# Performance work log

Measured on AMD Instinct MI355X. Metric: run time of the kernel, lower is better.

## Reference

```python
import jax, jax.numpy as jnp
import numpy as np
from jax import lax

DIM, HEADS, BS, TOPK, WIN = 256, 8, 8, 4, 7
HID = 2 * DIM  # DBFFN ffn_expansion_factor=2
B, H, W = 2, 56, 56


def _lin(x, w, b=None):
    # torch Linear: y = x @ W.T + b, W is [out, in]
    y = jnp.einsum('...c,oc->...o', x, w)
    return y if b is None else y + b


def _ln(x, w, b, eps=1e-6):
    mu = jnp.mean(x, -1, keepdims=True)
    var = jnp.mean((x - mu) ** 2, -1, keepdims=True)
    return (x - mu) * lax.rsqrt(var + eps) * w + b


def _mha(Q, K, V, wq_w, wq_b, wk_w, wk_b, wv_w, wv_b, p_w, p_b):
    # standard cross MHA: Q [B,Nq,C], K/V [B,Nk,C]
    Bq, Nq, C = Q.shape
    h, d = HEADS, C // HEADS
    scale = d ** -0.5
    q = _lin(Q, wq_w, wq_b).reshape(Bq, Nq, h, d)
    k = _lin(K, wk_w, wk_b).reshape(Bq, -1, h, d)
    v = _lin(V, wv_w, wv_b).reshape(Bq, -1, h, d)
    attn = jax.nn.softmax(jnp.einsum('bnhd,bmhd->bhnm', q, k) * scale, axis=-1)
    out = jnp.einsum('bhnm,bmhd->bnhd', attn, v).reshape(Bq, Nq, C)
    return _lin(out, p_w, p_b)


def setup_inputs() -> dict:
    key = jax.random.key(0)
    ks = jax.random.split(key, 16)
    s = 0.02
    C = DIM
    inp = {
        'x': jax.random.normal(ks[0], (B, C, H, W), jnp.float32),
        'pos_w': jax.random.normal(ks[1], (C, 1, 3, 3), jnp.float32) * s,
        'pos_b': jnp.zeros((C,), jnp.float32),
        'n1_w': jnp.ones((C,), jnp.float32), 'n1_b': jnp.zeros((C,), jnp.float32),
        'n2_w': jnp.ones((C,), jnp.float32), 'n2_b': jnp.zeros((C,), jnp.float32),
        'wq_w': jax.random.normal(ks[2], (3, C, C), jnp.float32) * s,
        'wq_b': jnp.zeros((3, C), jnp.float32),
        'wk_w': jax.random.normal(ks[3], (3, C, C), jnp.float32) * s,
        'wk_b': jnp.zeros((3, C), jnp.float32),
        'wv_w': jax.random.normal(ks[4], (3, C, C), jnp.float32) * s,
        'wv_b': jnp.zeros((3, C), jnp.float32),
        'pj_w': jax.random.normal(ks[5], (3, C, C), jnp.float32) * s,
        'pj_b': jnp.zeros((3, C), jnp.float32),
        # block scorer
        's1_w': jax.random.normal(ks[6], (C // 2, C), jnp.float32) * s,
        's1_b': jnp.zeros((C // 2,), jnp.float32),
        's2_w': jax.random.normal(ks[7], (1, C // 2), jnp.float32) * s,
        's2_b': jnp.zeros((1,), jnp.float32),
        # gating: per-token softmax weights over 3 branches
        'g_w': jax.random.normal(ks[8], (3, C), jnp.float32) * s,
        'g_b': jnp.zeros((3,), jnp.float32),
        # DBFFN (gated dconv FFN, bias=False): in-proj C->2*HID, dw 3x3, out-proj HID->C
        'pin_w': jax.random.normal(ks[9], (2 * HID, C), jnp.float32) * s,
        'dw_w': jax.random.normal(ks[10], (3, 3, 1, 2 * HID), jnp.float32) * s,
        'pout_w': jax.random.normal(ks[11], (C, HID), jnp.float32) * s,
    }
    return inp


def _forward(x, pos_w, pos_b, n1_w, n1_b, n2_w, n2_b, wq_w, wq_b, wk_w, wk_b,
             wv_w, wv_b, pj_w, pj_b, s1_w, s1_b, s2_w, s2_b, g_w, g_b,
             pin_w, dw_w, pout_w):
    Bx, C, Hx, Wx = x.shape
    # depthwise positional conv
    pos = lax.conv_general_dilated(x, pos_w, (1, 1), 'SAME',
                                   dimension_numbers=('NCHW', 'OIHW', 'NCHW'),
                                   feature_group_count=C)
    x = x + pos + pos_b[None, :, None, None] * 0 + pos_b[None, :, None, None]
    feat = jnp.transpose(x, (0, 2, 3, 1))  # NHWC
    Nq = Hx * Wx
    Q = feat.reshape(Bx, Nq, C)
    # block means
    nH, nW = Hx // BS, Wx // BS
    nB = nH * nW
    blk = feat.reshape(Bx, nH, BS, nW, BS, C).transpose(0, 1, 3, 2, 4, 5)
    blk = blk.reshape(Bx, nB, BS * BS, C).mean(axis=2)  # [B,nB,C]
    # block scores + top-k selection
    hsc = jax.nn.gelu(_lin(blk, s1_w, s1_b), approximate=False)
    scores = _lin(hsc, s2_w, s2_b)[..., 0]  # [B,nB]
    topk = min(TOPK, nB)
    _, idx = lax.top_k(scores, topk)
    K_sel = jnp.take_along_axis(blk, idx[:, :, None], axis=1)  # [B,topk,C]
    # compressed + selected branches
    y_cmp = _mha(Q, blk, blk, wq_w[0], wq_b[0], wk_w[0], wk_b[0], wv_w[0], wv_b[0], pj_w[0], pj_b[0])
    y_sel = _mha(Q, K_sel, K_sel, wq_w[1], wq_b[1], wk_w[1], wk_b[1], wv_w[1], wv_b[1], pj_w[1], pj_b[1])
    # local window branch (replicate-pad + unfold == shifted slices)
    pad = WIN // 2
    padded = jnp.pad(feat, ((0, 0), (pad, pad), (pad, pad), (0, 0)), mode='edge')
    patches = jnp.stack([padded[:, dy:dy + Hx, dx:dx + Wx, :]
                         for dy in range(WIN) for dx in range(WIN)], axis=3)
    patches = patches.reshape(Bx, Nq, WIN * WIN, C)  # [B,Nq,49,C]
    h, d = HEADS, C // HEADS
    scale = d ** -0.5
    q = _lin(Q, wq_w[2], wq_b[2]).reshape(Bx, Nq, h, d)
    k = _lin(patches, wk_w[2], wk_b[2]).reshape(Bx, Nq, WIN * WIN, h, d)
    v = _lin(patches, wv_w[2], wv_b[2]).reshape(Bx, Nq, WIN * WIN, h, d)
    attn = jax.nn.softmax(jnp.einsum('bnhd,bnwhd->bnhw', q, k) * scale, axis=-1)
    y_win = jnp.einsum('bnhw,bnwhd->bnhd', attn, v).reshape(Bx, Nq, C)
    y_win = _lin(y_win, pj_w[2], pj_b[2])
    # gated fusion + residual
    qn = _ln(Q, n1_w, n1_b)
    g = jax.nn.softmax(_lin(qn, g_w, g_b), axis=-1)  # [B,Nq,3]
    y = g[..., 0:1] * y_cmp + g[..., 1:2] * y_sel + g[..., 2:3] * y_win + Q
    ym = y.reshape(Bx, Hx, Wx, C)
    # DBFFN: gated depthwise-conv FFN (bias-free)
    t = _lin(ym, pin_w)  # [B,H,W,2*HID]
    t = lax.conv_general_dilated(t, dw_w, (1, 1), 'SAME',
                                 dimension_numbers=('NHWC', 'HWIO', 'NHWC'),
                                 feature_group_count=2 * HID)
    x1, x2 = jnp.split(t, 2, axis=-1)
    mlp = _lin(jax.nn.gelu(x1, approximate=False) * x2, pout_w)
    ym = _ln(ym + mlp, n2_w, n2_b)
    return jnp.transpose(ym, (0, 3, 1, 2))  # NCHW


def reference(x, pos_w, pos_b, n1_w, n1_b, n2_w, n2_b, wq_w, wq_b, wk_w, wk_b,
              wv_w, wv_b, pj_w, pj_b, s1_w, s1_b, s2_w, s2_b, g_w, g_b,
              pin_w, dw_w, pout_w):
    return _forward(x, pos_w, pos_b, n1_w, n1_b, n2_w, n2_b, wq_w, wq_b, wk_w,
                    wk_b, wv_w, wv_b, pj_w, pj_b, s1_w, s1_b, s2_w, s2_b,
                    g_w, g_b, pin_w, dw_w, pout_w)
```

## Files before the change

kernel.cpp:

```cpp
#include <hip/hip_runtime.h>

#define BATCH 2
#define CDIM 256
#define HEADS 8
#define HD 32
#define HH 56
#define WW 56
#define NQ 3136
#define NTOK 6272
#define NB 49
#define NTOPK 4
#define HID2 1024
#define HIDM 512
#define QSTRH 1280
#define ASTR 768

typedef short bf16x8 __attribute__((ext_vector_type(8)));
typedef float f32x4 __attribute__((ext_vector_type(4)));
typedef _Float16 h2 __attribute__((ext_vector_type(2)));
typedef _Float16 h4 __attribute__((ext_vector_type(4)));
struct __align__(16) h2x4 { h2 x, y, z, w; };

__device__ __forceinline__ float gelu_exact(float x) {
    return 0.5f * x * (1.f + erff(x * 0.70710678118654752f));
}

__device__ __forceinline__ short f2bf(float f) {
    union { float f; unsigned u; } v; v.f = f;
    unsigned r = v.u + 0x7FFFu + ((v.u >> 16) & 1u);
    return (short)(r >> 16);
}

__device__ __forceinline__ float fdot2h(h2 a, h2 b, float c) {
#if __has_builtin(__builtin_amdgcn_fdot2)
    return __builtin_amdgcn_fdot2(a, b, c, false);
#else
    return c + (float)a[0] * (float)b[0] + (float)a[1] * (float)b[1];
#endif
}

__device__ __forceinline__ void gld16(const void* gsrc, void* ldst) {
    __builtin_amdgcn_global_load_lds(
        (const __attribute__((address_space(1))) void*)gsrc,
        (__attribute__((address_space(3))) void*)ldst, 16, 0, 0);
}

__global__ __launch_bounds__(256) void k_init(
        const float* __restrict__ x, float* __restrict__ xT,
        const float* __restrict__ wq_w, const float* __restrict__ wk_w,
        const float* __restrict__ wv_w, const float* __restrict__ wq_b,
        const float* __restrict__ wk_b, const float* __restrict__ wv_b,
        const float* __restrict__ pj_w, const float* __restrict__ pin_w,
        const float* __restrict__ pout_w,
        short* __restrict__ Wc1, short* __restrict__ Wpj,
        short* __restrict__ Wpin, short* __restrict__ Wpout,
        float* __restrict__ bias1, float* __restrict__ Wkv0,
        float* __restrict__ bkv0, float* __restrict__ Wkv1,
        float* __restrict__ bkv1) {
    __shared__ float t[64][65];
    int bid = blockIdx.x;
    int tid = threadIdx.x;
    if (bid < 392) {
        int p0 = (bid % 49) * 64;
        int c0 = ((bid / 49) & 3) * 64;
        int b  = bid / 196;
        int pi = tid & 63, cj = tid >> 6;
        #pragma unroll
        for (int j = 0; j < 16; j++) {
            int c = cj * 16 + j;
            t[c][pi] = x[((size_t)(b * CDIM + c0 + c)) * NQ + p0 + pi];
        }
        __syncthreads();
        int ci = tid & 63, pj = tid >> 6;
        #pragma unroll
        for (int j = 0; j < 16; j++) {
            int p = pj * 16 + j;
            xT[((size_t)(b * NQ + p0 + p)) * CDIM + c0 + ci] = t[ci][p];
        }
        return;
    }
    int i = (bid - 392) * 256 + tid;
    if (i < 327680) {
        int r = i >> 8, k = i & 255, seg = r >> 8, n = r & 255;
        float v;
        if (seg == 0)      v = wq_w[n * 256 + k];
        else if (seg == 1) v = wq_w[65536 + n * 256 + k];
        else if (seg == 2) v = wq_w[131072 + n * 256 + k];
        else if (seg == 3) v = wk_w[131072 + n * 256 + k];
        else               v = wv_w[131072 + n * 256 + k];
        Wc1[i] = f2bf(v);
    } else if (i < 524288) {
        int j = i - 327680;
        int n = j / 768, tt = j % 768, br = tt >> 8, k = tt & 255;
        Wpj[j] = f2bf(pj_w[br * 65536 + n * 256 + k]);
    } else if (i < 786432) {
        int j = i - 524288;
        int r = j >> 8, k = j & 255;
        int o = (r & 3) * 256 + (r >> 2);
        Wpin[j] = f2bf(pin_w[o * 256 + k]);
    } else if (i < 917504) {
        int j = i - 786432;
        Wpout[j] = f2bf(pout_w[j]);
    } else if (i < 1048576) {
        int j = i - 917504;
        int r = j >> 8, k = j & 255;
        Wkv0[j] = (r < 256) ? wk_w[r * 256 + k] : wv_w[(r - 256) * 256 + k];
    } else if (i < 1179648) {
        int j = i - 1048576;
        int r = j >> 8, k = j & 255;
        Wkv1[j] = (r < 256) ? wk_w[65536 + r * 256 + k] : wv_w[65536 + (r - 256) * 256 + k];
    } else if (i < 1180928) {
        int j = i - 1179648;
        float v;
        if (j < 768)       v = wq_b[j];
        else if (j < 1024) v = wk_b[512 + (j - 768)];
        else               v = wv_b[512 + (j - 1024)];
        bias1[j] = v;
    } else if (i < 1181440) {
        int j = i - 1180928;
        bkv0[j] = (j < 256) ? wk_b[j] : wv_b[j - 256];
    } else if (i < 1181952) {
        int j = i - 1181440;
        bkv1[j] = (j < 256) ? wk_b[256 + j] : wv_b[j];
    }
}

__global__ __launch_bounds__(256) void k_posgates(
        const float* __restrict__ xT, const float* __restrict__ pw,
        const float* __restrict__ pb, const float* __restrict__ n1w,
        const float* __restrict__ n1b, const float* __restrict__ gw,
        const float* __restrict__ gb, float* __restrict__ feat,
        float* __restrict__ g, short* __restrict__ featb) {
    int wvid = threadIdx.x >> 6;
    int lane = threadIdx.x & 63;
    int c4 = lane * 4;
    float pwv[4][9];
    #pragma unroll
    for (int j = 0; j < 4; j++)
        #pragma unroll
        for (int i = 0; i < 9; i++) pwv[j][i] = pw[(c4 + j) * 9 + i];
    float4 pbv = *(const float4*)(pb + c4);
    float4 w1 = *(const float4*)(n1w + c4);
    float4 b1 = *(const float4*)(n1b + c4);
    float4 gw0 = *(const float4*)(gw + c4);
    float4 gw1 = *(const float4*)(gw + CDIM + c4);
    float4 gw2 = *(const float4*)(gw + 2 * CDIM + c4);
    float gb0 = gb[0], gb1 = gb[1], gb2 = gb[2];
    int tbase = blockIdx.x * 16 + wvid * 4;
    for (int t = 0; t < 4; t++) {
        int bn = tbase + t;
        int b = bn / NQ, n = bn % NQ;
        int y = n / WW, x = n % WW;
        const float* xb = xT + (size_t)b * NQ * CDIM;
        float4 a = *(const float4*)(xb + (size_t)n * CDIM + c4);
        float acc0 = a.x + pbv.x, acc1 = a.y + pbv.y;
        float acc2 = a.z + pbv.z, acc3 = a.w + pbv.w;
        #pragma unroll
        for (int dy = 0; dy < 3; dy++) {
            int yy = y + dy - 1;
            if (yy < 0 || yy >= HH) continue;
            #pragma unroll
            for (int dx = 0; dx < 3; dx++) {
                int xx = x + dx - 1;
                if (xx < 0 || xx >= WW) continue;
                float4 v = *(const float4*)(xb + ((size_t)(yy * WW + xx)) * CDIM + c4);
                int wi = dy * 3 + dx;
                acc0 += v.x * pwv[0][wi];
                acc1 += v.y * pwv[1][wi];
                acc2 += v.z * pwv[2][wi];
                acc3 += v.w * pwv[3][wi];
            }
        }
        *(float4*)(feat + (size_t)bn * CDIM + c4) = make_float4(acc0, acc1, acc2, acc3);
        short4 fb;
        fb.x = f2bf(acc0); fb.y = f2bf(acc1); fb.z = f2bf(acc2); fb.w = f2bf(acc3);
        *(short4*)(featb + (size_t)bn * CDIM + c4) = fb;
        float s = acc0 + acc1 + acc2 + acc3;
        #pragma unroll
        for (int off = 32; off > 0; off >>= 1) s += __shfl_xor(s, off);
        float mu = s * (1.f / CDIM);
        float d0 = acc0 - mu, d1 = acc1 - mu, d2 = acc2 - mu, d3 = acc3 - mu;
        float ss = d0 * d0 + d1 * d1 + d2 * d2 + d3 * d3;
        #pragma unroll
        for (int off = 32; off > 0; off >>= 1) ss += __shfl_xor(ss, off);
        float rstd = rsqrtf(ss * (1.f / CDIM) + 1e-6f);
        float q0 = d0 * rstd * w1.x + b1.x;
        float q1 = d1 * rstd * w1.y + b1.y;
        float q2 = d2 * rstd * w1.z + b1.z;
        float q3 = d3 * rstd * w1.w + b1.w;
        float p0 = q0 * gw0.x + q1 * gw0.y + q2 * gw0.z + q3 * gw0.w;
        float p1 = q0 * gw1.x + q1 * gw1.y + q2 * gw1.z + q3 * gw1.w;
        float p2 = q0 * gw2.x + q1 * gw2.y + q2 * gw2.z + q3 * gw2.w;
        #pragma unroll
        for (int off = 32; off > 0; off >>= 1) {
            p0 += __shfl_xor(p0, off);
            p1 += __shfl_xor(p1, off);
            p2 += __shfl_xor(p2, off);
        }
        if (lane == 0) {
            float l0 = p0 + gb0, l1 = p1 + gb1, l2 = p2 + gb2;
            float m3 = fmaxf(l0, fmaxf(l1, l2));
            float e0 = __expf(l0 - m3), e1 = __expf(l1 - m3), e2 = __expf(l2 - m3);
            float inv = 1.f / (e0 + e1 + e2);
            g[bn * 3 + 0] = e0 * inv;
            g[bn * 3 + 1] = e1 * inv;
            g[bn * 3 + 2] = e2 * inv;
        }
    }
}

__global__ __launch_bounds__(256) void k_blkscore(
        const float* __restrict__ feat, const float* __restrict__ s1w,
        const float* __restrict__ s1b, const float* __restrict__ s2w,
        const float* __restrict__ s2b, float* __restrict__ blk,
        float* __restrict__ scores) {
    __shared__ float sblk[256];
    __shared__ float red[128];
    int gid = blockIdx.x;
    int b = gid / NB, bid = gid % NB;
    int by = bid / 7, bx = bid % 7;
    int c = threadIdx.x;
    float s = 0.f;
    for (int iy = 0; iy < 8; iy++)
        for (int ix = 0; ix < 8; ix++) {
            int y = by * 8 + iy, xx = bx * 8 + ix;
            s += feat[((size_t)(b * NQ + y * WW + xx)) * CDIM + c];
        }
    s *= (1.f / 64.f);
    blk[(size_t)gid * CDIM + c] = s;
    sblk[c] = s;
    __syncthreads();
    if (c < 128) {
        const float* wrow = s1w + (size_t)c * CDIM;
        float acc = s1b[c];
        for (int k = 0; k < CDIM; k++) acc += sblk[k] * wrow[k];
        red[c] = gelu_exact(acc) * s2w[c];
    }
    __syncthreads();
    #pragma unroll
    for (int st = 64; st > 0; st >>= 1) {
        if (c < st) red[c] += red[c + st];
        __syncthreads();
    }
    if (c == 0) scores[gid] = red[0] + s2b[0];
}

__global__ __launch_bounds__(256) void k_gemm64kv(
        const float* __restrict__ blk, const float* __restrict__ Wkv0,
        const float* __restrict__ bkv0, _Float16* __restrict__ kvcmp,
        const float* __restrict__ scores, const float* __restrict__ Wkv1,
        const float* __restrict__ bkv1, _Float16* __restrict__ kvsel) {
    __shared__ float As[16][68];
    __shared__ float Ws[16][68];
    __shared__ float ssc[2][NB];
    __shared__ int sidx[8];
    const float* W; const float* bias; _Float16* C; int M;
    int m0;
    bool sel = (blockIdx.y == 2);
    if (!sel) { W = Wkv0; bias = bkv0; C = kvcmp; M = 98; m0 = blockIdx.y * 64; }
    else      { W = Wkv1; bias = bkv1; C = kvsel; M = 8;  m0 = 0; }
    const int N = 512, K = 256;
    const int tid = threadIdx.x;
    const int tx = tid & 15, ty = tid >> 4;
    const int n0 = blockIdx.x * 64;
    const int lr = tid >> 2;
    const int lk = (tid & 3) * 4;
    if (sel) {
        if (tid < 2 * NB) ssc[tid / NB][tid % NB] = scores[tid];
        __syncthreads();
        if (tid < 2) {
            for (int t = 0; t < NTOPK; t++) {
                int best = 0; float bv = -1e30f;
                for (int m = 0; m < NB; m++)
                    if (ssc[tid][m] > bv) { bv = ssc[tid][m]; best = m; }
                sidx[tid * 4 + t] = best; ssc[tid][best] = -1e30f;
            }
        }
        __syncthreads();
    }
    int gm = m0 + lr;
    int arow = gm;
    if (sel && gm < 8) arow = (gm >> 2) * NB + sidx[gm];
    float acc[4][4] = {};
    for (int k0 = 0; k0 < K; k0 += 16) {
        float4 av = make_float4(0.f, 0.f, 0.f, 0.f);
        if (gm < M) av = *(const float4*)(blk + (size_t)arow * K + k0 + lk);
        int gn = n0 + lr;
        float4 wv = make_float4(0.f, 0.f, 0.f, 0.f);
        if (gn < N) wv = *(const float4*)(W + (size_t)gn * K + k0 + lk);
        __syncthreads();
        As[lk][lr] = av.x; As[lk + 1][lr] = av.y; As[lk + 2][lr] = av.z; As[lk + 3][lr] = av.w;
        Ws[lk][lr] = wv.x; Ws[lk + 1][lr] = wv.y; Ws[lk + 2][lr] = wv.z; Ws[lk + 3][lr] = wv.w;
        __syncthreads();
        #pragma unroll
        for (int kk = 0; kk < 16; kk++) {
            const float4 a = *(const float4*)&As[kk][ty * 4];
            const float4 b = *(const float4*)&Ws[kk][tx * 4];
            acc[0][0] += a.x * b.x; acc[0][1] += a.x * b.y; acc[0][2] += a.x * b.z; acc[0][3] += a.x * b.w;
            acc[1][0] += a.y * b.x; acc[1][1] += a.y * b.y; acc[1][2] += a.y * b.z; acc[1][3] += a.y * b.w;
            acc[2][0] += a.z * b.x; acc[2][1] += a.z * b.y; acc[2][2] += a.z * b.z; acc[2][3] += a.z * b.w;
            acc[3][0] += a.w * b.x; acc[3][1] += a.w * b.y; acc[3][2] += a.w * b.z; acc[3][3] += a.w * b.w;
        }
    }
    #pragma unroll
    for (int i = 0; i < 4; i++) {
        int om = m0 + ty * 4 + i;
        if (om >= M) break;
        #pragma unroll
        for (int j = 0; j < 4; j++) {
            int gn = n0 + tx * 4 + j;
            C[(size_t)om * N + gn] = (_Float16)(acc[i][j] + bias[gn]);
        }
    }
}

__global__ __launch_bounds__(256) void k_gemm64x128(
        const short* __restrict__ A, const short* __restrict__ W,
        const float* __restrict__ bias, int M, int N, int K,
        _Float16* __restrict__ C2) {
    __shared__ short As[64][40];
    __shared__ short Bs[128][40];
    int tid = threadIdx.x;
    int wid = tid >> 6, lane = tid & 63;
    int wm = wid >> 1, wn = wid & 1;
    int m0 = blockIdx.y * 64, n0 = blockIdx.x * 128;
    f32x4 acc[2][4] = {};
    int ar = tid >> 2, ac = (tid & 3) * 8;
    int br = tid >> 1, bc = (tid & 1) * 16;
    int fr = lane & 15, fk = (lane >> 4) * 8;
    for (int k0 = 0; k0 < K; k0 += 32) {
        bf16x8 a0 = *(const bf16x8*)(A + (size_t)(m0 + ar) * K + k0 + ac);
        const short* wp = W + (size_t)(n0 + br) * K + k0 + bc;
        bf16x8 wv0 = *(const bf16x8*)(wp);
        bf16x8 wv1 = *(const bf16x8*)(wp + 8);
        __syncthreads();
        *(bf16x8*)&As[ar][ac] = a0;
        *(bf16x8*)&Bs[br][bc] = wv0;
        *(bf16x8*)&Bs[br][bc + 8] = wv1;
        __syncthreads();
        bf16x8 af[2], bf[4];
        #pragma unroll
        for (int mi = 0; mi < 2; mi++)
            af[mi] = *(const bf16x8*)&As[wm * 32 + mi * 16 + fr][fk];
        #pragma unroll
        for (int ni = 0; ni < 4; ni++)
            bf[ni] = *(const bf16x8*)&Bs[wn * 64 + ni * 16 + fr][fk];
        #pragma unroll
        for (int mi = 0; mi < 2; mi++)
            #pragma unroll
            for (int ni = 0; ni < 4; ni++)
                acc[mi][ni] = __builtin_amdgcn_mfma_f32_16x16x32_bf16(
                    af[mi], bf[ni], acc[mi][ni], 0, 0, 0);
    }
    int rsub = (lane >> 4) * 4;
    #pragma unroll
    for (int mi = 0; mi < 2; mi++) {
        #pragma unroll
        for (int ni = 0; ni < 4; ni++) {
            int col = n0 + wn * 64 + ni * 16 + (lane & 15);
            float bv = bias ? bias[col] : 0.f;
            #pragma unroll
            for (int r = 0; r < 4; r++) {
                int row = m0 + wm * 32 + mi * 16 + rsub + r;
                C2[(size_t)row * N + col] = (_Float16)(acc[mi][ni][r] + bv);
            }
        }
    }
}

__global__ __launch_bounds__(256) void k_gemm64(
        const short* __restrict__ A, const short* __restrict__ W,
        const float* __restrict__ bias, float* __restrict__ C,
        int M, int N, int K,
        const float* __restrict__ resid, const float* __restrict__ g3,
        const float* __restrict__ pjb, short* __restrict__ Cb) {
    __shared__ short As[64][40];
    __shared__ short Bs[64][40];
    int tid = threadIdx.x;
    int wid = tid >> 6, lane = tid & 63;
    int wm = wid >> 1, wn = wid & 1;
    int m0 = blockIdx.y * 64, n0 = blockIdx.x * 64;
    f32x4 acc[2][2] = {};
    int ar = tid >> 2, ac = (tid & 3) * 8;
    int fr = lane & 15, fk = (lane >> 4) * 8;
    for (int k0 = 0; k0 < K; k0 += 32) {
        bf16x8 a0 = *(const bf16x8*)(A + (size_t)(m0 + ar) * K + k0 + ac);
        bf16x8 w0 = *(const bf16x8*)(W + (size_t)(n0 + ar) * K + k0 + ac);
        __syncthreads();
        *(bf16x8*)&As[ar][ac] = a0;
        *(bf16x8*)&Bs[ar][ac] = w0;
        __syncthreads();
        bf16x8 af[2], bf[2];
        #pragma unroll
        for (int mi = 0; mi < 2; mi++)
            af[mi] = *(const bf16x8*)&As[wm * 32 + mi * 16 + fr][fk];
        #pragma unroll
        for (int ni = 0; ni < 2; ni++)
            bf[ni] = *(const bf16x8*)&Bs[wn * 32 + ni * 16 + fr][fk];
        #pragma unroll
        for (int mi = 0; mi < 2; mi++)
            #pragma unroll
            for (int ni = 0; ni < 2; ni++)
                acc[mi][ni] = __builtin_amdgcn_mfma_f32_16x16x32_bf16(
                    af[mi], bf[ni], acc[mi][ni], 0, 0, 0);
    }
    int rsub = (lane >> 4) * 4;
    #pragma unroll
    for (int mi = 0; mi < 2; mi++) {
        #pragma unroll
        for (int ni = 0; ni < 2; ni++) {
            int col = n0 + wn * 32 + ni * 16 + (lane & 15);
            #pragma unroll
            for (int r = 0; r < 4; r++) {
                int row = m0 + wm * 32 + mi * 16 + rsub + r;
                float v = acc[mi][ni][r];
                if (resid) {
                    v += resid[(size_t)row * N + col]
                       + g3[row * 3 + 0] * pjb[col]
                       + g3[row * 3 + 1] * pjb[256 + col]
                       + g3[row * 3 + 2] * pjb[512 + col];
                } else if (bias) {
                    v += bias[col];
                }
                C[(size_t)row * N + col] = v;
                if (Cb) Cb[(size_t)row * N + col] = f2bf(v);
            }
        }
    }
}

__global__ __launch_bounds__(512) void k_attn_lds(
        const _Float16* __restrict__ bufQ, const _Float16* __restrict__ kvc,
        const _Float16* __restrict__ kvs, short* __restrict__ Acatb,
        const float* __restrict__ g) {
    __shared__ uint4 buf[100 * 32];
    int tid = threadIdx.x;
    int wid = tid >> 6;
    int lane = tid & 63;
    int l = tid & 31;
    int tk = tid >> 5;
    int dg = l & 3;
    int co = l * 8;
    const float scale = 0.17677669529663687f;

    if (blockIdx.x < 392) {
        int bid = blockIdx.x;
        int swz = (bid & 7) * 49 + (bid >> 3);
        int t0 = swz * 16;
        int tok = t0 + tk;
        int b = t0 / NQ;
        const _Float16* kb = kvc + (size_t)b * NB * 512;
        for (int p = wid * 2; p < NB + 1; p += 16) {
            int myp = p + (lane >> 5);
            if (myp > NB - 1) myp = NB - 1;
            gld16((const uint4*)(kb + (size_t)myp * 512) + (lane & 31), &buf[p * 32]);
        }
        const _Float16* qrow = bufQ + (size_t)tok * QSTRH;
        float gate0 = g[tok * 3 + 0];
        float gate1 = g[tok * 3 + 1];
        short* orow = Acatb + (size_t)tok * ASTR;
        h2x4 qv = *(const h2x4*)(qrow + co);
        __syncthreads();
        float sc[13];
        sc[12] = -1e30f;
        #pragma unroll
        for (int m = 0; m < NB; m++) {
            h2x4 kv = *(const h2x4*)&buf[m * 32 + l];
            float acc = fdot2h(qv.x, kv.x, 0.f);
            acc = fdot2h(qv.y, kv.y, acc);
            acc = fdot2h(qv.z, kv.z, acc);
            acc = fdot2h(qv.w, kv.w, acc);
            acc += __shfl_xor(acc, 1);
            acc += __shfl_xor(acc, 2);
            if ((m & 3) == dg) sc[m >> 2] = acc * scale;
        }
        float mx = sc[0];
        #pragma unroll
        for (int i = 1; i < 13; i++) mx = fmaxf(mx, sc[i]);
        mx = fmaxf(mx, __shfl_xor(mx, 1));
        mx = fmaxf(mx, __shfl_xor(mx, 2));
        float sum = 0.f;
        #pragma unroll
        for (int i = 0; i < 13; i++) { sc[i] = __expf(sc[i] - mx); sum += sc[i]; }
        sum += __shfl_xor(sum, 1);
        sum += __shfl_xor(sum, 2);
        float inv_c = 1.f / sum;
        __syncthreads();
        for (int p = wid * 2; p < NB + 1; p += 16) {
            int myp = p + (lane >> 5);
            if (myp > NB - 1) myp = NB - 1;
            gld16((const uint4*)(kb + (size_t)myp * 512 + 256) + (lane & 31), &buf[p * 32]);
        }
        {
            const _Float16* ksb = kvs + (size_t)b * NTOPK * 512;
            h2x4 qs = *(const h2x4*)(qrow + 256 + co);
            float sv = 0.f;
            #pragma unroll
            for (int m = 0; m < NTOPK; m++) {
                h2x4 kk = *(const h2x4*)(ksb + (size_t)m * 512 + co);
                float acc = fdot2h(qs.x, kk.x, 0.f);
                acc = fdot2h(qs.y, kk.y, acc);
                acc = fdot2h(qs.z, kk.z, acc);
                acc = fdot2h(qs.w, kk.w, acc);
                acc += __shfl_xor(acc, 1);
                acc += __shfl_xor(acc, 2);
                if (m == dg) sv = acc * scale;
            }
            float mxs = sv;
            mxs = fmaxf(mxs, __shfl_xor(mxs, 1));
            mxs = fmaxf(mxs, __shfl_xor(mxs, 2));
            float e = __expf(sv - mxs);
            float sums = e;
            sums += __shfl_xor(sums, 1);
            sums += __shfl_xor(sums, 2);
            float invs = 1.f / sums;
            float o[8];
            #pragma unroll
            for (int d = 0; d < 8; d++) o[d] = 0.f;
            #pragma unroll
            for (int m = 0; m < NTOPK; m++) {
                float pw = __shfl(e, m, 4);
                h2x4 vv = *(const h2x4*)(ksb + (size_t)m * 512 + 256 + co);
                o[0] += pw * (float)vv.x[0]; o[1] += pw * (float)vv.x[1];
                o[2] += pw * (float)vv.y[0]; o[3] += pw * (float)vv.y[1];
                o[4] += pw * (float)vv.z[0]; o[5] += pw * (float)vv.z[1];
                o[6] += pw * (float)vv.w[0]; o[7] += pw * (float)vv.w[1];
            }
            float gg = gate1 * invs;
            bf16x8 ov;
            #pragma unroll
            for (int d = 0; d < 8; d++) ov[d] = f2bf(o[d] * gg);
            *(bf16x8*)(orow + 256 + co) = ov;
        }
        __syncthreads();
        {
            float o[8];
            #pragma unroll
            for (int d = 0; d < 8; d++) o[d] = 0.f;
            #pragma unroll
            for (int m = 0; m < NB; m++) {
                float pw = __shfl(sc[m >> 2], m & 3, 4);
                h2x4 vv = *(const h2x4*)&buf[m * 32 + l];
                o[0] += pw * (float)vv.x[0]; o[1] += pw * (float)vv.x[1];
                o[2] += pw * (float)vv.y[0]; o[3] += pw * (float)vv.y[1];
                o[4] += pw * (float)vv.z[0]; o[5] += pw * (float)vv.z[1];
                o[6] += pw * (float)vv.w[0]; o[7] += pw * (float)vv.w[1];
            }
            float gg = gate0 * inv_c;
            bf16x8 ov;
            #pragma unroll
            for (int d = 0; d < 8; d++) ov[d] = f2bf(o[d] * gg);
            *(bf16x8*)(orow + co) = ov;
        }
    } else {
        int bid = blockIdx.x - 392;
        int swz = (bid & 7) * 49 + (bid >> 3);
        int b = swz / 196;
        int r = swz % 196;
        int y0 = (r / 14) * 4;
        int x0 = (r % 14) * 4;
        int ty = tk >> 2, tx = tk & 3;
        int y = y0 + ty, x = x0 + tx;
        int tok = b * NQ + y * WW + x;
        const _Float16* KVb = bufQ + (size_t)b * NQ * QSTRH;
        for (int p = wid * 2; p < 100; p += 16) {
            int pp = p + (lane >> 5);
            int pr = pp / 10, pc = pp - pr * 10;
            int gy = min(max(y0 + pr - 3, 0), HH - 1);
            int gx = min(max(x0 + pc - 3, 0), WW - 1);
            gld16((const uint4*)(KVb + (size_t)(gy * WW + gx) * QSTRH + 768) + (lane & 31),
                  &buf[p * 32]);
        }
        h2x4 qv = *(const h2x4*)(bufQ + (size_t)tok * QSTRH + 512 + co);
        float gate = g[tok * 3 + 2];
        __syncthreads();
        float sw[13];
        sw[12] = -1e30f;
        #pragma unroll
        for (int dy = 0; dy < 7; dy++) {
            #pragma unroll
            for (int dx = 0; dx < 7; dx++) {
                int p = (ty + dy) * 10 + tx + dx;
                h2x4 kv = *(const h2x4*)&buf[p * 32 + l];
                float acc = fdot2h(qv.x, kv.x, 0.f);
                acc = fdot2h(qv.y, kv.y, acc);
                acc = fdot2h(qv.z, kv.z, acc);
                acc = fdot2h(qv.w, kv.w, acc);
                acc += __shfl_xor(acc, 1);
                acc += __shfl_xor(acc, 2);
                int m = dy * 7 + dx;
                if ((m & 3) == dg) sw[m >> 2] = acc * scale;
            }
        }
        float mx = sw[0];
        #pragma unroll
        for (int i = 1; i < 13; i++) mx = fmaxf(mx, sw[i]);
        mx = fmaxf(mx, __shfl_xor(mx, 1));
        mx = fmaxf(mx, __shfl_xor(mx, 2));
        float sum = 0.f;
        #pragma unroll
        for (int i = 0; i < 13; i++) { sw[i] = __expf(sw[i] - mx); sum += sw[i]; }
        sum += __shfl_xor(sum, 1);
        sum += __shfl_xor(sum, 2);
        float inv = 1.f / sum;
        __syncthreads();
        for (int p = wid * 2; p < 100; p += 16) {
            int pp = p + (lane >> 5);
            int pr = pp / 10, pc = pp - pr * 10;
            int gy = min(max(y0 + pr - 3, 0), HH - 1);
            int gx = min(max(x0 + pc - 3, 0), WW - 1);
            gld16((const uint4*)(KVb + (size_t)(gy * WW + gx) * QSTRH + 1024) + (lane & 31),
                  &buf[p * 32]);
        }
        __syncthreads();
        float o[8];
        #pragma unroll
        for (int d = 0; d < 8; d++) o[d] = 0.f;
        #pragma unroll
        for (int dy = 0; dy < 7; dy++) {
            #pragma unroll
            for (int dx = 0; dx < 7; dx++) {
                int p = (ty + dy) * 10 + tx + dx;
                int m = dy * 7 + dx;
                float pw = __shfl(sw[m >> 2], m & 3, 4);
                h2x4 vv = *(const h2x4*)&buf[p * 32 + l];
                o[0] += pw * (float)vv.x[0]; o[1] += pw * (float)vv.x[1];
                o[2] += pw * (float)vv.y[0]; o[3] += pw * (float)vv.y[1];
                o[4] += pw * (float)vv.z[0]; o[5] += pw * (float)vv.z[1];
                o[6] += pw * (float)vv.w[0]; o[7] += pw * (float)vv.w[1];
            }
        }
        float gg = gate * inv;
        short* op = Acatb + (size_t)tok * ASTR + 512 + co;
        bf16x8 ov;
        #pragma unroll
        for (int d = 0; d < 8; d++) ov[d] = f2bf(o[d] * gg);
        *(bf16x8*)(op) = ov;
    }
}

__global__ __launch_bounds__(256) void k_dwglu2(
        const _Float16* __restrict__ t, const float* __restrict__ w,
        short* __restrict__ G) {
    int gid = blockIdx.x;
    int xq = gid & 7;
    int y = (gid >> 3) % HH;
    int b = gid / (HH * 8);
    int c = threadIdx.x;
    float wv[9][4];
    #pragma unroll
    for (int i = 0; i < 9; i++)
        #pragma unroll
        for (int j = 0; j < 4; j++) wv[i][j] = w[i * HID2 + j * 256 + c];
    const _Float16* tb = t + (size_t)b * NQ * HID2;
    short* Gbase = G + (size_t)b * NQ * HIDM;
    int x0 = xq * 7;
    float col[3][3][4];
    #pragma unroll
    for (int ci = 0; ci < 2; ci++) {
        int xx = x0 - 1 + ci;
        #pragma unroll
        for (int r = 0; r < 3; r++) {
            int yy = y + r - 1;
            bool ok = (xx >= 0) && (yy >= 0) && (yy < HH);
            h4 v = {};
            if (ok) v = *(const h4*)(tb + ((size_t)(yy * WW + xx)) * HID2 + c * 4);
            #pragma unroll
            for (int j = 0; j < 4; j++) col[ci][r][j] = (float)v[j];
        }
    }
    #pragma unroll
    for (int i = 0; i < 7; i++) {
        int xx = x0 + i;
        {
            int xl = xx + 1;
            #pragma unroll
            for (int r = 0; r < 3; r++) {
                int yy = y + r - 1;
                bool ok = (xl < WW) && (yy >= 0) && (yy < HH);
                h4 v = {};
                if (ok) v = *(const h4*)(tb + ((size_t)(yy * WW + xl)) * HID2 + c * 4);
                #pragma unroll
                for (int j = 0; j < 4; j++) col[(i + 2) % 3][r][j] = (float)v[j];
            }
        }
        float a0 = 0.f, a1 = 0.f, a2 = 0.f, a3 = 0.f;
        #pragma unroll
        for (int r = 0; r < 3; r++) {
            #pragma unroll
            for (int dxx = 0; dxx < 3; dxx++) {
                const float* cc = col[(i + dxx) % 3][r];
                int wi = r * 3 + dxx;
                a0 += cc[0] * wv[wi][0];
                a1 += cc[1] * wv[wi][1];
                a2 += cc[2] * wv[wi][2];
                a3 += cc[3] * wv[wi][3];
            }
        }
        short* Gb = Gbase + (size_t)(y * WW + xx) * HIDM;
        Gb[c]       = f2bf(gelu_exact(a0) * a2);
        Gb[c + 256] = f2bf(gelu_exact(a1) * a3);
    }
}

__global__ __launch_bounds__(256) void k_lntr(
        const float* __restrict__ ym, const float* __restrict__ mlp,
        const float* __restrict__ n2w, const float* __restrict__ n2b,
        float* __restrict__ out) {
    __shared__ float t[32][257];
    int bx = blockIdx.x;
    int b = bx / 98;
    int p0 = (bx % 98) * 32;
    int tid = threadIdx.x;
    int wv = tid >> 6, lane = tid & 63;
    int c4 = lane * 4;
    float4 w = *(const float4*)(n2w + c4);
    float4 bb = *(const float4*)(n2b + c4);
    #pragma unroll
    for (int i = 0; i < 8; i++) {
        int p = wv * 8 + i;
        size_t base = ((size_t)(b * NQ + p0 + p)) * CDIM + c4;
        float4 a = *(const float4*)(ym + base);
        float4 m = *(const float4*)(mlp + base);
        float v0 = a.x + m.x, v1 = a.y + m.y, v2 = a.z + m.z, v3 = a.w + m.w;
        float s = v0 + v1 + v2 + v3;
        #pragma unroll
        for (int off = 32; off > 0; off >>= 1) s += __shfl_xor(s, off);
        float mu = s * (1.f / CDIM);
        float d0 = v0 - mu, d1 = v1 - mu, d2 = v2 - mu, d3 = v3 - mu;
        float ss = d0 * d0 + d1 * d1 + d2 * d2 + d3 * d3;
        #pragma unroll
        for (int off = 32; off > 0; off >>= 1) ss += __shfl_xor(ss, off);
        float rstd = rsqrtf(ss * (1.f / CDIM) + 1e-6f);
        t[p][c4 + 0] = d0 * rstd * w.x + bb.x;
        t[p][c4 + 1] = d1 * rstd * w.y + bb.y;
        t[p][c4 + 2] = d2 * rstd * w.z + bb.z;
        t[p][c4 + 3] = d3 * rstd * w.w + bb.w;
    }
    __syncthreads();
    int pi = tid & 31, cg = tid >> 5;
    #pragma unroll
    for (int j = 0; j < 32; j++) {
        int c = cg * 32 + j;
        out[((size_t)(b * CDIM + c)) * NQ + p0 + pi] = t[pi][c];
    }
}

extern "C" void kernel_launch(void* const* d_in, const int* in_sizes, int n_in,
                              void* d_out, int out_size, void* d_ws, size_t ws_size,
                              hipStream_t stream) {
    const float* x     = (const float*)d_in[0];
    const float* pos_w = (const float*)d_in[1];
    const float* pos_b = (const float*)d_in[2];
    const float* n1w   = (const float*)d_in[3];
    const float* n1b   = (const float*)d_in[4];
    const float* n2w   = (const float*)d_in[5];
    const float* n2b   = (const float*)d_in[6];
    const float* wq_w  = (const float*)d_in[7];
    const float* wq_b  = (const float*)d_in[8];
    const float* wk_w  = (const float*)d_in[9];
    const float* wk_b  = (const float*)d_in[10];
    const float* wv_w  = (const float*)d_in[11];
    const float* wv_b  = (const float*)d_in[12];
    const float* pj_w  = (const float*)d_in[13];
    const float* pj_b  = (const float*)d_in[14];
    const float* s1w   = (const float*)d_in[15];
    const float* s1b   = (const float*)d_in[16];
    const float* s2w   = (const float*)d_in[17];
    const float* s2b   = (const float*)d_in[18];
    const float* gw    = (const float*)d_in[19];
    const float* gb    = (const float*)d_in[20];
    const float* pinw  = (const float*)d_in[21];
    const float* dww   = (const float*)d_in[22];
    const float* poutw = (const float*)d_in[23];
    float* out = (float*)d_out;
    float* ws  = (float*)d_ws;

    const size_t SZ = (size_t)NTOK * CDIM;
    float* feat = ws;
    _Float16* bufQh = (_Float16*)(feat + SZ);
    float* R1   = (float*)(bufQh + (size_t)NTOK * QSTRH);
    float* xT   = R1;
    short* Acatb = (short*)R1;
    _Float16* T1h = (_Float16*)R1;
    float* ym   = R1 + (size_t)NTOK * 512;
    short* featb = (short*)(ym + SZ);
    short* ymb   = featb + (size_t)NTOK * CDIM;
    float* blk   = (float*)(ymb + (size_t)NTOK * CDIM);
    _Float16* kvcmp = (_Float16*)(blk + 98 * 256);
    _Float16* kvsel = kvcmp + 98 * 512;
    float* scores = (float*)(kvsel + 8 * 512);
    float* g      = scores + 128;
    float* bias1  = g + (size_t)NTOK * 3;
    float* Wkv0   = bias1 + 1280;
    float* bkv0   = Wkv0 + 512 * 256;
    float* Wkv1   = bkv0 + 512;
    float* bkv1   = Wkv1 + 512 * 256;
    short* Wc1    = (short*)(bkv1 + 512);
    short* Wpj    = Wc1 + 1280 * 256;
    short* Wpin   = Wpj + 256 * 768;
    short* Wpout  = Wpin + 1024 * 256;
    short* G      = (short*)bufQh;
    float* MLP    = (float*)(bufQh + (size_t)NTOK * 512);

    hipLaunchKernelGGL(k_init, dim3(392 + 4618), dim3(256), 0, stream,
                       x, xT, wq_w, wk_w, wv_w, wq_b, wk_b, wv_b, pj_w, pinw, poutw,
                       Wc1, Wpj, Wpin, Wpout, bias1, Wkv0, bkv0, Wkv1, bkv1);
    hipLaunchKernelGGL(k_posgates, dim3(NTOK / 16), dim3(256), 0, stream,
                       xT, pos_w, pos_b, n1w, n1b, gw, gb, feat, g, featb);
    hipLaunchKernelGGL(k_blkscore, dim3(BATCH * NB), dim3(256), 0, stream,
                       feat, s1w, s1b, s2w, s2b, blk, scores);
    hipLaunchKernelGGL(k_gemm64kv, dim3(8, 3), dim3(256), 0, stream,
                       blk, Wkv0, bkv0, kvcmp, scores, Wkv1, bkv1, kvsel);
    hipLaunchKernelGGL(k_gemm64x128, dim3(1280 / 128, NTOK / 64), dim3(256), 0, stream,
                       featb, Wc1, bias1, NTOK, 1280, 256, bufQh);
    hipLaunchKernelGGL(k_attn_lds, dim3(784), dim3(512), 0, stream,
                       bufQh, kvcmp, kvsel, Acatb, g);
    hipLaunchKernelGGL(k_gemm64, dim3(CDIM / 64, NTOK / 64), dim3(256), 0, stream,
                       Acatb, Wpj, nullptr, ym, NTOK, CDIM, ASTR, feat, g, pj_b, ymb);
    hipLaunchKernelGGL(k_gemm64x128, dim3(HID2 / 128, NTOK / 64), dim3(256), 0, stream,
                       ymb, Wpin, nullptr, NTOK, HID2, 256, T1h);
    hipLaunchKernelGGL(k_dwglu2, dim3(BATCH * HH * 8), dim3(256), 0, stream, T1h, dww, G);
    hipLaunchKernelGGL(k_gemm64, dim3(CDIM / 64, NTOK / 64), dim3(256), 0, stream,
                       G, Wpout, nullptr, MLP, NTOK, CDIM, HIDM,
                       nullptr, nullptr, nullptr, (short*)nullptr);
    hipLaunchKernelGGL(k_lntr, dim3(196), dim3(256), 0, stream, ym, MLP, n2w, n2b, out);
}
```

Measured before the change: 166.9 us.

## Fuse output projection GEMM with residual LayerNorm and transpose; widen GEMM K-tile

Adds a kernel that computes the pout GEMM for 32 tokens across all 256 channels, adds the residual, runs LayerNorm through cross-wave shared reductions and writes NCHW output directly. This removes the fp32 MLP intermediate round trip and one launch. Separately, both generic GEMMs now stage 64-wide K tiles per sync instead of 32, halving barrier count. The fused kernel reads weights straight from global memory per wave without LDS staging, which may raise load traffic.

```diff
diff --git a/kernel.cpp b/kernel.cpp
--- a/kernel.cpp
+++ b/kernel.cpp
@@ -318,39 +318,49 @@
         const short* __restrict__ A, const short* __restrict__ W,
         const float* __restrict__ bias, int M, int N, int K,
         _Float16* __restrict__ C2) {
-    __shared__ short As[64][40];
-    __shared__ short Bs[128][40];
+    __shared__ short As[64][72];
+    __shared__ short Bs[128][72];
     int tid = threadIdx.x;
     int wid = tid >> 6, lane = tid & 63;
     int wm = wid >> 1, wn = wid & 1;
     int m0 = blockIdx.y * 64, n0 = blockIdx.x * 128;
     f32x4 acc[2][4] = {};
-    int ar = tid >> 2, ac = (tid & 3) * 8;
-    int br = tid >> 1, bc = (tid & 1) * 16;
+    int ar = tid >> 2, ac = (tid & 3) * 16;
+    int br = tid >> 1, bc = (tid & 1) * 32;
     int fr = lane & 15, fk = (lane >> 4) * 8;
-    for (int k0 = 0; k0 < K; k0 += 32) {
-        bf16x8 a0 = *(const bf16x8*)(A + (size_t)(m0 + ar) * K + k0 + ac);
+    for (int k0 = 0; k0 < K; k0 += 64) {
+        const short* ap = A + (size_t)(m0 + ar) * K + k0 + ac;
+        bf16x8 a0 = *(const bf16x8*)(ap);
+        bf16x8 a1 = *(const bf16x8*)(ap + 8);
         const short* wp = W + (size_t)(n0 + br) * K + k0 + bc;
-        bf16x8 wv0 = *(const bf16x8*)(wp);
-        bf16x8 wv1 = *(const bf16x8*)(wp + 8);
+        bf16x8 w0 = *(const bf16x8*)(wp);
+        bf16x8 w1 = *(const bf16x8*)(wp + 8);
+        bf16x8 w2 = *(const bf16x8*)(wp + 16);
+        bf16x8 w3 = *(const bf16x8*)(wp + 24);
         __syncthreads();
         *(bf16x8*)&As[ar][ac] = a0;
-        *(bf16x8*)&Bs[br][bc] = wv0;
-        *(bf16x8*)&Bs[br][bc + 8] = wv1;
-        __syncthreads();
-        bf16x8 af[2], bf[4];
-        #pragma unroll
-        for (int mi = 0; mi < 2; mi++)
-            af[mi] = *(const bf16x8*)&As[wm * 32 + mi * 16 + fr][fk];
-        #pragma unroll
-        for (int ni = 0; ni < 4; ni++)
-            bf[ni] = *(const bf16x8*)&Bs[wn * 64 + ni * 16 + fr][fk];
-        #pragma unroll
-        for (int mi = 0; mi < 2; mi++)
+        *(bf16x8*)&As[ar][ac + 8] = a1;
+        *(bf16x8*)&Bs[br][bc] = w0;
+        *(bf16x8*)&Bs[br][bc + 8] = w1;
+        *(bf16x8*)&Bs[br][bc + 16] = w2;
+        *(bf16x8*)&Bs[br][bc + 24] = w3;
+        __syncthreads();
+        #pragma unroll
+        for (int kk = 0; kk < 64; kk += 32) {
+            bf16x8 af[2], bf[4];
+            #pragma unroll
+            for (int mi = 0; mi < 2; mi++)
+                af[mi] = *(const bf16x8*)&As[wm * 32 + mi * 16 + fr][kk + fk];
             #pragma unroll
             for (int ni = 0; ni < 4; ni++)
-                acc[mi][ni] = __builtin_amdgcn_mfma_f32_16x16x32_bf16(
-                    af[mi], bf[ni], acc[mi][ni], 0, 0, 0);
+                bf[ni] = *(const bf16x8*)&Bs[wn * 64 + ni * 16 + fr][kk + fk];
+            #pragma unroll
+            for (int mi = 0; mi < 2; mi++)
+                #pragma unroll
+                for (int ni = 0; ni < 4; ni++)
+                    acc[mi][ni] = __builtin_amdgcn_mfma_f32_16x16x32_bf16(
+                        af[mi], bf[ni], acc[mi][ni], 0, 0, 0);
+        }
     }
     int rsub = (lane >> 4) * 4;
     #pragma unroll
@@ -374,35 +384,44 @@
         int M, int N, int K,
         const float* __restrict__ resid, const float* __restrict__ g3,
         const float* __restrict__ pjb, short* __restrict__ Cb) {
-    __shared__ short As[64][40];
-    __shared__ short Bs[64][40];
+    __shared__ short As[64][72];
+    __shared__ short Bs[64][72];
     int tid = threadIdx.x;
     int wid = tid >> 6, lane = tid & 63;
     int wm = wid >> 1, wn = wid & 1;
     int m0 = blockIdx.y * 64, n0 = blockIdx.x * 64;
     f32x4 acc[2][2] = {};
-    int ar = tid >> 2, ac = (tid & 3) * 8;
+    int ar = tid >> 2, ac = (tid & 3) * 16;
     int fr = lane & 15, fk = (lane >> 4) * 8;
-    for (int k0 = 0; k0 < K; k0 += 32) {
-        bf16x8 a0 = *(const bf16x8*)(A + (size_t)(m0 + ar) * K + k0 + ac);
-        bf16x8 w0 = *(const bf16x8*)(W + (size_t)(n0 + ar) * K + k0 + ac);
+    for (int k0 = 0; k0 < K; k0 += 64) {
+        const short* ap = A + (size_t)(m0 + ar) * K + k0 + ac;
+        bf16x8 a0 = *(const bf16x8*)(ap);
+        bf16x8 a1 = *(const bf16x8*)(ap + 8);
+        const short* wp = W + (size_t)(n0 + ar) * K + k0 + ac;
+        bf16x8 w0 = *(const bf16x8*)(wp);
+        bf16x8 w1 = *(const bf16x8*)(wp + 8);
         __syncthreads();
         *(bf16x8*)&As[ar][ac] = a0;
+        *(bf16x8*)&As[ar][ac + 8] = a1;
         *(bf16x8*)&Bs[ar][ac] = w0;
-        __syncthreads();
-        bf16x8 af[2], bf[2];
-        #pragma unroll
-        for (int mi = 0; mi < 2; mi++)
-            af[mi] = *(const bf16x8*)&As[wm * 32 + mi * 16 + fr][fk];
-        #pragma unroll
-        for (int ni = 0; ni < 2; ni++)
-            bf[ni] = *(const bf16x8*)&Bs[wn * 32 + ni * 16 + fr][fk];
-        #pragma unroll
-        for (int mi = 0; mi < 2; mi++)
+        *(bf16x8*)&Bs[ar][ac + 8] = w1;
+        __syncthreads();
+        #pragma unroll
+        for (int kk = 0; kk < 64; kk += 32) {
+            bf16x8 af[2], bf[2];
+            #pragma unroll
+            for (int mi = 0; mi < 2; mi++)
+                af[mi] = *(const bf16x8*)&As[wm * 32 + mi * 16 + fr][kk + fk];
             #pragma unroll
             for (int ni = 0; ni < 2; ni++)
-                acc[mi][ni] = __builtin_amdgcn_mfma_f32_16x16x32_bf16(
-                    af[mi], bf[ni], acc[mi][ni], 0, 0, 0);
+                bf[ni] = *(const bf16x8*)&Bs[wn * 32 + ni * 16 + fr][kk + fk];
+            #pragma unroll
+            for (int mi = 0; mi < 2; mi++)
+                #pragma unroll
+                for (int ni = 0; ni < 2; ni++)
+                    acc[mi][ni] = __builtin_amdgcn_mfma_f32_16x16x32_bf16(
+                        af[mi], bf[ni], acc[mi][ni], 0, 0, 0);
+        }
     }
     int rsub = (lane >> 4) * 4;
     #pragma unroll
@@ -425,6 +444,118 @@
                 C[(size_t)row * N + col] = v;
                 if (Cb) Cb[(size_t)row * N + col] = f2bf(v);
             }
+        }
+    }
+}
+
+__global__ __launch_bounds__(256) void k_poutln(
+        const short* __restrict__ G, const short* __restrict__ W,
+        const float* __restrict__ ym, const float* __restrict__ n2w,
+        const float* __restrict__ n2b, float* __restrict__ out) {
+    __shared__ short As[32][72];
+    __shared__ float redS[4][36];
+    __shared__ float redQ[4][36];
+    int tid = threadIdx.x;
+    int wid = tid >> 6, lane = tid & 63;
+    int bx = blockIdx.x;
+    int b = bx / 98;
+    int t0g = bx * 32;
+    int p0 = (bx % 98) * 32;
+    f32x4 acc[2][4] = {};
+    int ar = tid >> 3, ac = (tid & 7) * 8;
+    int fr = lane & 15, fk = (lane >> 4) * 8;
+    const short* Wb = W + (size_t)(wid * 64) * 512;
+    for (int k0 = 0; k0 < 512; k0 += 64) {
+        bf16x8 a0 = *(const bf16x8*)(G + (size_t)(t0g + ar) * 512 + k0 + ac);
+        __syncthreads();
+        *(bf16x8*)&As[ar][ac] = a0;
+        __syncthreads();
+        #pragma unroll
+        for (int kk = 0; kk < 64; kk += 32) {
+            bf16x8 af[2], bf[4];
+            #pragma unroll
+            for (int mi = 0; mi < 2; mi++)
+                af[mi] = *(const bf16x8*)&As[mi * 16 + fr][kk + fk];
+            #pragma unroll
+            for (int ni = 0; ni < 4; ni++)
+                bf[ni] = *(const bf16x8*)(Wb + (size_t)(ni * 16 + fr) * 512 + k0 + kk + fk);
+            #pragma unroll
+            for (int mi = 0; mi < 2; mi++)
+                #pragma unroll
+                for (int ni = 0; ni < 4; ni++)
+                    acc[mi][ni] = __builtin_amdgcn_mfma_f32_16x16x32_bf16(
+                        af[mi], bf[ni], acc[mi][ni], 0, 0, 0);
+        }
+    }
+    int rsub = (lane >> 4) * 4;
+    float v[2][4][4];
+    #pragma unroll
+    for (int mi = 0; mi < 2; mi++)
+        #pragma unroll
+        for (int ni = 0; ni < 4; ni++) {
+            int col = wid * 64 + ni * 16 + fr;
+            #pragma unroll
+            for (int r = 0; r < 4; r++) {
+                int row = mi * 16 + rsub + r;
+                v[mi][ni][r] = acc[mi][ni][r] + ym[(size_t)(t0g + row) * CDIM + col];
+            }
+        }
+    #pragma unroll
+    for (int mi = 0; mi < 2; mi++) {
+        #pragma unroll
+        for (int r = 0; r < 4; r++) {
+            float s = v[mi][0][r] + v[mi][1][r] + v[mi][2][r] + v[mi][3][r];
+            s += __shfl_xor(s, 1); s += __shfl_xor(s, 2);
+            s += __shfl_xor(s, 4); s += __shfl_xor(s, 8);
+            if (fr == 0) redS[wid][mi * 16 + rsub + r] = s;
+        }
+    }
+    __syncthreads();
+    float mu[2][4];
+    #pragma unroll
+    for (int mi = 0; mi < 2; mi++)
+        #pragma unroll
+        for (int r = 0; r < 4; r++) {
+            int row = mi * 16 + rsub + r;
+            mu[mi][r] = (redS[0][row] + redS[1][row] + redS[2][row] + redS[3][row])
+                        * (1.f / CDIM);
+        }
+    #pragma unroll
+    for (int mi = 0; mi < 2; mi++) {
+        #pragma unroll
+        for (int r = 0; r < 4; r++) {
+            float m = mu[mi][r];
+            float d0 = v[mi][0][r] - m, d1 = v[mi][1][r] - m;
+            float d2 = v[mi][2][r] - m, d3 = v[mi][3][r] - m;
+            float q = d0 * d0 + d1 * d1 + d2 * d2 + d3 * d3;
+            q += __shfl_xor(q, 1); q += __shfl_xor(q, 2);
+            q += __shfl_xor(q, 4); q += __shfl_xor(q, 8);
+            if (fr == 0) redQ[wid][mi * 16 + rsub + r] = q;
+        }
+    }
+    __syncthreads();
+    float rstd[2][4];
+    #pragma unroll
+    for (int mi = 0; mi < 2; mi++)
+        #pragma unroll
+        for (int r = 0; r < 4; r++) {
+            int row = mi * 16 + rsub + r;
+            float var = (redQ[0][row] + redQ[1][row] + redQ[2][row] + redQ[3][row])
+                        * (1.f / CDIM);
+            rstd[mi][r] = rsqrtf(var + 1e-6f);
+        }
+    #pragma unroll
+    for (int mi = 0; mi < 2; mi++) {
+        #pragma unroll
+        for (int ni = 0; ni < 4; ni++) {
+            int col = wid * 64 + ni * 16 + fr;
+            float wgt = n2w[col], bia = n2b[col];
+            float4 o;
+            o.x = (v[mi][ni][0] - mu[mi][0]) * rstd[mi][0] * wgt + bia;
+            o.y = (v[mi][ni][1] - mu[mi][1]) * rstd[mi][1] * wgt + bia;
+            o.z = (v[mi][ni][2] - mu[mi][2]) * rstd[mi][2] * wgt + bia;
+            o.w = (v[mi][ni][3] - mu[mi][3]) * rstd[mi][3] * wgt + bia;
+            *(float4*)(out + ((size_t)(b * CDIM + col)) * NQ + p0 + mi * 16 + rsub) = o;
         }
     }
 }
@@ -700,49 +831,6 @@
         short* Gb = Gbase + (size_t)(y * WW + xx) * HIDM;
         Gb[c]       = f2bf(gelu_exact(a0) * a2);
         Gb[c + 256] = f2bf(gelu_exact(a1) * a3);
-    }
-}
-
-__global__ __launch_bounds__(256) void k_lntr(
-        const float* __restrict__ ym, const float* __restrict__ mlp,
-        const float* __restrict__ n2w, const float* __restrict__ n2b,
-        float* __restrict__ out) {
-    __shared__ float t[32][257];
-    int bx = blockIdx.x;
-    int b = bx / 98;
-    int p0 = (bx % 98) * 32;
-    int tid = threadIdx.x;
-    int wv = tid >> 6, lane = tid & 63;
-    int c4 = lane * 4;
-    float4 w = *(const float4*)(n2w + c4);
-    float4 bb = *(const float4*)(n2b + c4);
-    #pragma unroll
-    for (int i = 0; i < 8; i++) {
-        int p = wv * 8 + i;
-        size_t base = ((size_t)(b * NQ + p0 + p)) * CDIM + c4;
-        float4 a = *(const float4*)(ym + base);
-        float4 m = *(const float4*)(mlp + base);
-        float v0 = a.x + m.x, v1 = a.y + m.y, v2 = a.z + m.z, v3 = a.w + m.w;
-        float s = v0 + v1 + v2 + v3;
-        #pragma unroll
-        for (int off = 32; off > 0; off >>= 1) s += __shfl_xor(s, off);
-        float mu = s * (1.f / CDIM);
-        float d0 = v0 - mu, d1 = v1 - mu, d2 = v2 - mu, d3 = v3 - mu;
-        float ss = d0 * d0 + d1 * d1 + d2 * d2 + d3 * d3;
-        #pragma unroll
-        for (int off = 32; off > 0; off >>= 1) ss += __shfl_xor(ss, off);
-        float rstd = rsqrtf(ss * (1.f / CDIM) + 1e-6f);
-        t[p][c4 + 0] = d0 * rstd * w.x + bb.x;
-        t[p][c4 + 1] = d1 * rstd * w.y + bb.y;
-        t[p][c4 + 2] = d2 * rstd * w.z + bb.z;
-        t[p][c4 + 3] = d3 * rstd * w.w + bb.w;
-    }
-    __syncthreads();
-    int pi = tid & 31, cg = tid >> 5;
-    #pragma unroll
-    for (int j = 0; j < 32; j++) {
-        int c = cg * 32 + j;
-        out[((size_t)(b * CDIM + c)) * NQ + p0 + pi] = t[pi][c];
     }
 }
 
@@ -801,7 +889,6 @@
     short* Wpin   = Wpj + 256 * 768;
     short* Wpout  = Wpin + 1024 * 256;
     short* G      = (short*)bufQh;
-    float* MLP    = (float*)(bufQh + (size_t)NTOK * 512);
 
     hipLaunchKernelGGL(k_init, dim3(392 + 4618), dim3(256), 0, stream,
                        x, xT, wq_w, wk_w, wv_w, wq_b, wk_b, wv_b, pj_w, pinw, poutw,
@@ -821,8 +908,6 @@
     hipLaunchKernelGGL(k_gemm64x128, dim3(HID2 / 128, NTOK / 64), dim3(256), 0, stream,
                        ymb, Wpin, nullptr, NTOK, HID2, 256, T1h);
     hipLaunchKernelGGL(k_dwglu2, dim3(BATCH * HH * 8), dim3(256), 0, stream, T1h, dww, G);
-    hipLaunchKernelGGL(k_gemm64, dim3(CDIM / 64, NTOK / 64), dim3(256), 0, stream,
-                       G, Wpout, nullptr, MLP, NTOK, CDIM, HIDM,
-                       nullptr, nullptr, nullptr, (short*)nullptr);
-    hipLaunchKernelGGL(k_lntr, dim3(196), dim3(256), 0, stream, ym, MLP, n2w, n2b, out);
-}
+    hipLaunchKernelGGL(k_poutln, dim3(NTOK / 32), dim3(256), 0, stream,
+                       G, Wpout, ym, n2w, n2b, out);
+}
```

Result: faster. 162.6 us (-2.6%).
